# Performance work log

Measured on AMD Instinct MI355X. Metric: run time of the kernel, lower is better.

## Reference

```python
import jax, jax.numpy as jnp
import numpy as np

EPS = 1e-12  # matches torch F.normalize eps


def setup_inputs() -> dict:
    key = jax.random.key(0)
    k1, k2, k3, k4 = jax.random.split(key, 4)
    B, T, C, E, I = 2, 2048, 1024, 16, 256
    return {
        "hidden_states": jax.random.normal(k1, (B, T, C), dtype=jnp.float32),
        "sim_matrix": jax.random.normal(k2, (C, E), dtype=jnp.float32),
        "threshold": jnp.zeros((1,), dtype=jnp.float32),
        "W1": jax.random.normal(k3, (E, I, C), dtype=jnp.float32) * (C ** -0.5),
        "W2": jax.random.normal(k4, (E, C, I), dtype=jnp.float32) * (I ** -0.5),
    }


def reference(hidden_states, sim_matrix, threshold, W1, W2):
    B, T, C = hidden_states.shape
    x = hidden_states.reshape(-1, C)  # [N, C]
    # gate: cosine-similarity scores, threshold mask
    xn = x / jnp.maximum(jnp.linalg.norm(x, axis=-1, keepdims=True), EPS)
    sn = sim_matrix / jnp.maximum(jnp.linalg.norm(sim_matrix, axis=0, keepdims=True), EPS)
    scores = xn @ sn                      # [N, E]
    mask = scores > threshold             # [N, E] bool
    k_per_token = mask.sum(axis=-1)       # [N]
    # expert FFNs: dense per-expert GEMMs, then mask (equals sparse dispatch + zero-fill)
    h = jax.nn.gelu(jnp.einsum('tc,eic->tei', x, W1), approximate=False)  # [N, E, I]
    out = jnp.einsum('tei,eci->tec', h, W2)                               # [N, E, C]
    expert_outputs_full = jnp.where(mask[..., None], out, 0.0)            # [N, E, C]
    # STE gate forward value is just the mask; combine = masked sum over experts
    ste = mask.astype(scores.dtype)
    final = (expert_outputs_full * ste[..., None]).sum(axis=1)            # [N, C]
    return final.reshape(B, T, C), scores, expert_outputs_full, k_per_token
```

## Files before the change

kernel.cpp:

```cpp
#include <hip/hip_runtime.h>
#include <hip/hip_bf16.h>
#include <math.h>
#include <stdint.h>

#define N_TOK 4096
#define C_DIM 1024
#define E_NUM 16
#define I_DIM 256

typedef unsigned short ushort_t;
typedef __attribute__((ext_vector_type(8))) short bf16x8;
typedef __attribute__((ext_vector_type(4))) float f32x4;

#define AS1 __attribute__((address_space(1)))
#define AS3 __attribute__((address_space(3)))

__device__ __forceinline__ void glds16(const void* g, void* l) {
    __builtin_amdgcn_global_load_lds((const AS1 uint32_t*)g, (AS3 uint32_t*)l, 16, 0, 0);
}

__device__ __forceinline__ ushort_t bf16_rne(float v) {
    uint32_t u = __float_as_uint(v);
    u = (u + 0x7FFFu + ((u >> 16) & 1u)) >> 16;
    return (ushort_t)u;
}
__device__ __forceinline__ float bf16_val(ushort_t h) {
    return __uint_as_float(((uint32_t)h) << 16);
}
__device__ __forceinline__ float gelu_exact(float v) {
    return 0.5f * v * (1.0f + erff(v * 0.70710678118654752f));
}

__global__ __launch_bounds__(256) void smk_split(
    const float* __restrict__ src, char* __restrict__ dst, int R, int kush)
{
    const int u  = blockIdx.x * 256 + threadIdx.x;
    const int ku = 1 << kush;
    const int r  = u >> kush;
    const int k8 = u & (ku - 1);
    const int p  = k8 >> 2;
    const int uh = (k8 & 3) ^ (r & 7);

    const float* s = src + ((size_t)r << (kush + 3)) + k8 * 8;
    float4 a = *(const float4*)(s);
    float4 b = *(const float4*)(s + 4);
    float f[8] = {a.x, a.y, a.z, a.w, b.x, b.y, b.z, b.w};

    uint4 hi4, lo4;
    ushort_t* hp = (ushort_t*)&hi4;
    ushort_t* lp = (ushort_t*)&lo4;
    #pragma unroll
    for (int j = 0; j < 8; ++j) {
        ushort_t h = bf16_rne(f[j]);
        hp[j] = h;
        lp[j] = bf16_rne(f[j] - bf16_val(h));
    }
    size_t ob = (((size_t)p * R + r) * 8 + uh) * 16;
    *(uint4*)(dst + ob)        = hi4;
    *(uint4*)(dst + (ob ^ 64)) = lo4;
}

__global__ __launch_bounds__(256) void smk_splitBH(
    const float* __restrict__ src, char* __restrict__ dst, int R, int kush)
{
    const int u  = blockIdx.x * 256 + threadIdx.x;
    const int ku = 1 << kush;
    const int r  = u >> kush;
    const int k8 = u & (ku - 1);
    const int p  = k8 >> 2;
    const int q  = p >> 1;
    const int uh = ((k8 & 3) | ((p & 1) << 2)) ^ (r & 7);

    const float* s = src + ((size_t)r << (kush + 3)) + k8 * 8;
    float4 a = *(const float4*)(s);
    float4 b = *(const float4*)(s + 4);
    float f[8] = {a.x, a.y, a.z, a.w, b.x, b.y, b.z, b.w};

    uint4 hi4;
    ushort_t* hp = (ushort_t*)&hi4;
    #pragma unroll
    for (int j = 0; j < 8; ++j) hp[j] = bf16_rne(f[j]);

    *(uint4*)(dst + (((size_t)q * R + r) * 8 + uh) * 16) = hi4;
}

__global__ __launch_bounds__(256) void smk_gate2(
    const float* __restrict__ x, const float* __restrict__ sim,
    const float* __restrict__ thr,
    float* __restrict__ scores, float* __restrict__ kpt)
{
    __shared__ __align__(16) float ss[C_DIM * E_NUM];
    __shared__ float pm[16][17];
    __shared__ float inv_ns[E_NUM];
    __shared__ float mrow[16][17];

    const int tid = threadIdx.x;
    #pragma unroll
    for (int q = 0; q < 16; ++q)
        *(float4*)&ss[q * 1024 + tid * 4] = *(const float4*)&sim[q * 1024 + tid * 4];
    __syncthreads();

    const int e = tid & 15;
    const int g = tid >> 4;
    float ps = 0.f;
    for (int c = g; c < C_DIM; c += 16) {
        float v = ss[c * 16 + e];
        ps = fmaf(v, v, ps);
    }
    pm[g][e] = ps;
    __syncthreads();
    if (tid < 16) {
        float s = 0.f;
        #pragma unroll
        for (int gg = 0; gg < 16; ++gg) s += pm[gg][tid];
        inv_ns[tid] = 1.f / fmaxf(sqrtf(s), 1e-12f);
    }
    __syncthreads();

    const int t = blockIdx.x * 16 + g;
    const float* xr = x + (size_t)t * C_DIM;
    float dot = 0.f, sq = 0.f;
    for (int c = 0; c < C_DIM; c += 4) {
        float4 xv = *(const float4*)&xr[c];
        dot = fmaf(xv.x, ss[(c + 0) * 16 + e], dot);
        dot = fmaf(xv.y, ss[(c + 1) * 16 + e], dot);
        dot = fmaf(xv.z, ss[(c + 2) * 16 + e], dot);
        dot = fmaf(xv.w, ss[(c + 3) * 16 + e], dot);
        sq  = fmaf(xv.x, xv.x, sq); sq = fmaf(xv.y, xv.y, sq);
        sq  = fmaf(xv.z, xv.z, sq); sq = fmaf(xv.w, xv.w, sq);
    }
    float sc = dot * inv_ns[e] * (1.f / fmaxf(sqrtf(sq), 1e-12f));
    scores[(size_t)t * E_NUM + e] = sc;
    mrow[g][e] = (sc > thr[0]) ? 1.f : 0.f;
    __syncthreads();
    if (e == 0) {
        float k = 0.f;
        #pragma unroll
        for (int ee = 0; ee < 16; ++ee) k += mrow[g][ee];
        kpt[t] = k;
    }
}

__global__ __launch_bounds__(256) void smk_ffn1_mfma(
    const char* __restrict__ Xs, const char* __restrict__ W1h,
    char* __restrict__ Hsh)
{
    __shared__ char As[16384];
    __shared__ char Bs[16384];

    const int e  = blockIdx.z;
    const int t0 = blockIdx.x * 128;
    const int i0 = blockIdx.y * 128;
    const int tid  = threadIdx.x;
    const int lane = tid & 63;
    const int w    = tid >> 6;
    const int wr   = w >> 1, wc = w & 1;

    f32x4 acc[4][4];
    #pragma unroll
    for (int mi = 0; mi < 4; ++mi)
        #pragma unroll
        for (int ni = 0; ni < 4; ++ni)
            acc[mi][ni] = (f32x4){0.f, 0.f, 0.f, 0.f};

    const char* Ag = Xs  + (size_t)t0 * 128 + tid * 16;
    const char* Bg = W1h + ((size_t)(e * 256) + i0) * 128 + tid * 16;

    for (int p = 0; p < 32; ++p) {
        __syncthreads();
        const char* ga = Ag + (size_t)p * (4096 * 128);
        #pragma unroll
        for (int q = 0; q < 4; ++q)
            glds16(ga + q * 4096, As + q * 4096 + tid * 16);
        if ((p & 1) == 0) {
            const char* gb = Bg + (size_t)(p >> 1) * (4096 * 128);
            #pragma unroll
            for (int q = 0; q < 4; ++q)
                glds16(gb + q * 4096, Bs + q * 4096 + tid * 16);
        }
        __syncthreads();

        bf16x8 ah[4], al[4], bh[4];
        #pragma unroll
        for (int mi = 0; mi < 4; ++mi) {
            int r   = wr * 64 + mi * 16 + (lane & 15);
            int ubh = (((lane >> 4)    ) ^ (r & 7)) * 16;
            int ubl = (((lane >> 4) | 4) ^ (r & 7)) * 16;
            ah[mi] = *(const bf16x8*)(As + r * 128 + ubh);
            al[mi] = *(const bf16x8*)(As + r * 128 + ubl);
        }
        const int ubsel = (lane >> 4) | ((p & 1) << 2);
        #pragma unroll
        for (int ni = 0; ni < 4; ++ni) {
            int r  = wc * 64 + ni * 16 + (lane & 15);
            int ub = (ubsel ^ (r & 7)) * 16;
            bh[ni] = *(const bf16x8*)(Bs + r * 128 + ub);
        }
        #pragma unroll
        for (int mi = 0; mi < 4; ++mi)
            #pragma unroll
            for (int ni = 0; ni < 4; ++ni) {
                acc[mi][ni] = __builtin_amdgcn_mfma_f32_16x16x32_bf16(ah[mi], bh[ni], acc[mi][ni], 0, 0, 0);
                acc[mi][ni] = __builtin_amdgcn_mfma_f32_16x16x32_bf16(al[mi], bh[ni], acc[mi][ni], 0, 0, 0);
            }
    }

    const int rb = (lane >> 4) * 4;
    #pragma unroll
    for (int mi = 0; mi < 4; ++mi)
        #pragma unroll
        for (int ni = 0; ni < 4; ++ni) {
            int ig = i0 + wc * 64 + ni * 16 + (lane & 15);
            int pp = ig >> 5, qq = pp >> 1;
            int uu = ((ig >> 3) & 3) | ((pp & 1) << 2);
            #pragma unroll
            for (int j = 0; j < 4; ++j) {
                int t = t0 + wr * 64 + mi * 16 + rb + j;
                float v = gelu_exact(acc[mi][ni][j]);
                size_t ob = (((size_t)((e * 4 + qq) * 4096 + t)) * 8 + (uu ^ (t & 7))) * 16
                          + (ig & 7) * 2;
                *(ushort_t*)(Hsh + ob) = bf16_rne(v);
            }
        }
}

__global__ __launch_bounds__(256) void smk_ffn2_mfma(
    const char* __restrict__ Hsh, const char* __restrict__ W2s,
    const float* __restrict__ scores, const float* __restrict__ thr,
    float* __restrict__ eo)
{
    __shared__ char As[16384];
    __shared__ char Bs[16384];

    const int e  = blockIdx.z;
    const int t0 = blockIdx.x * 128;
    const int c0 = blockIdx.y * 128;
    const int tid  = threadIdx.x;
    const int lane = tid & 63;
    const int w    = tid >> 6;
    const int wr   = w >> 1, wc = w & 1;

    f32x4 acc[4][4];
    #pragma unroll
    for (int mi = 0; mi < 4; ++mi)
        #pragma unroll
        for (int ni = 0; ni < 4; ++ni)
            acc[mi][ni] = (f32x4){0.f, 0.f, 0.f, 0.f};

    const char* Ag = Hsh + ((size_t)(e * 4) * 4096 + t0) * 128 + tid * 16;
    const char* Bg = W2s + ((size_t)(e * 1024) + c0) * 128 + tid * 16;

    for (int p = 0; p < 8; ++p) {
        __syncthreads();
        if ((p & 1) == 0) {
            const char* ga = Ag + (size_t)(p >> 1) * (4096 * 128);
            #pragma unroll
            for (int q = 0; q < 4; ++q)
                glds16(ga + q * 4096, As + q * 4096 + tid * 16);
        }
        const char* gb = Bg + (size_t)p * (16384 * 128);
        #pragma unroll
        for (int q = 0; q < 4; ++q)
            glds16(gb + q * 4096, Bs + q * 4096 + tid * 16);
        __syncthreads();

        bf16x8 ah[4], bh[4], bl[4];
        const int uasel = (lane >> 4) | ((p & 1) << 2);
        #pragma unroll
        for (int mi = 0; mi < 4; ++mi) {
            int r  = wr * 64 + mi * 16 + (lane & 15);
            int ua = (uasel ^ (r & 7)) * 16;
            ah[mi] = *(const bf16x8*)(As + r * 128 + ua);
        }
        #pragma unroll
        for (int ni = 0; ni < 4; ++ni) {
            int r   = wc * 64 + ni * 16 + (lane & 15);
            int ubh = (((lane >> 4)    ) ^ (r & 7)) * 16;
            int ubl = (((lane >> 4) | 4) ^ (r & 7)) * 16;
            bh[ni] = *(const bf16x8*)(Bs + r * 128 + ubh);
            bl[ni] = *(const bf16x8*)(Bs + r * 128 + ubl);
        }
        #pragma unroll
        for (int mi = 0; mi < 4; ++mi)
            #pragma unroll
            for (int ni = 0; ni < 4; ++ni) {
                acc[mi][ni] = __builtin_amdgcn_mfma_f32_16x16x32_bf16(ah[mi], bh[ni], acc[mi][ni], 0, 0, 0);
                acc[mi][ni] = __builtin_amdgcn_mfma_f32_16x16x32_bf16(ah[mi], bl[ni], acc[mi][ni], 0, 0, 0);
            }
    }

    const float th = thr[0];
    const int rb = (lane >> 4) * 4;
    float msk[4][4];
    #pragma unroll
    for (int mi = 0; mi < 4; ++mi)
        #pragma unroll
        for (int j = 0; j < 4; ++j) {
            int t = t0 + wr * 64 + mi * 16 + rb + j;
            msk[mi][j] = (scores[(size_t)t * E_NUM + e] > th) ? 1.f : 0.f;
        }
    #pragma unroll
    for (int mi = 0; mi < 4; ++mi)
        #pragma unroll
        for (int ni = 0; ni < 4; ++ni) {
            int c = c0 + wc * 64 + ni * 16 + (lane & 15);
            #pragma unroll
            for (int j = 0; j < 4; ++j) {
                int t = t0 + wr * 64 + mi * 16 + rb + j;
                eo[((size_t)t * E_NUM + e) * C_DIM + c] = acc[mi][ni][j] * msk[mi][j];
            }
        }
}

__global__ __launch_bounds__(256) void smk_combine(
    const float* __restrict__ eo, float* __restrict__ fin)
{
    size_t idx = ((size_t)blockIdx.x * 256 + threadIdx.x) * 4;
    size_t t = idx / C_DIM;
    int c = (int)(idx % C_DIM);
    const float* p = eo + (size_t)t * E_NUM * C_DIM + c;
    float4 s = {0.f, 0.f, 0.f, 0.f};
    #pragma unroll
    for (int e = 0; e < E_NUM; ++e) {
        float4 v = *(const float4*)&p[(size_t)e * C_DIM];
        s.x += v.x; s.y += v.y; s.z += v.z; s.w += v.w;
    }
    *(float4*)&fin[idx] = s;
}

#define BM 64
#define BN 64
#define KC 16
#define LDP 68

__global__ __launch_bounds__(256) void smk_ffn1(
    const float* __restrict__ X, const float* __restrict__ W1,
    float* __restrict__ H, int eh, int ez0)
{
    const int e  = blockIdx.z + ez0;
    const int t0 = blockIdx.x * BM;
    const int i0 = blockIdx.y * BN;
    const float* Ap = X + (size_t)t0 * C_DIM;
    const float* Bp = W1 + ((size_t)e * I_DIM + i0) * C_DIM;
    __shared__ __align__(16) float As[KC][LDP];
    __shared__ __align__(16) float Bs[KC][LDP];
    const int tid = threadIdx.x;
    const int tx = tid & 15, ty = tid >> 4;
    const int lm = tid >> 2;
    const int lk = (tid & 3) * 4;
    float acc[4][4] = {};
    for (int k0 = 0; k0 < C_DIM; k0 += KC) {
        float4 av = *(const float4*)&Ap[(size_t)lm * C_DIM + k0 + lk];
        float4 bv = *(const float4*)&Bp[(size_t)lm * C_DIM + k0 + lk];
        __syncthreads();
        As[lk + 0][lm] = av.x; As[lk + 1][lm] = av.y;
        As[lk + 2][lm] = av.z; As[lk + 3][lm] = av.w;
        Bs[lk + 0][lm] = bv.x; Bs[lk + 1][lm] = bv.y;
        Bs[lk + 2][lm] = bv.z; Bs[lk + 3][lm] = bv.w;
        __syncthreads();
        #pragma unroll
        for (int k = 0; k < KC; ++k) {
            float4 a4 = *(const float4*)&As[k][ty * 4];
            float4 b4 = *(const float4*)&Bs[k][tx * 4];
            float a[4] = {a4.x, a4.y, a4.z, a4.w};
            float b[4] = {b4.x, b4.y, b4.z, b4.w};
            #pragma unroll
            for (int i = 0; i < 4; ++i)
                #pragma unroll
                for (int j = 0; j < 4; ++j)
                    acc[i][j] = fmaf(a[i], b[j], acc[i][j]);
        }
    }
    const size_t hrow = (size_t)eh * I_DIM;
    float* Hp = H + ((eh == E_NUM) ? (size_t)e * I_DIM : 0);
    #pragma unroll
    for (int i = 0; i < 4; ++i) {
        int t = t0 + ty * 4 + i;
        float4 o;
        o.x = gelu_exact(acc[i][0]); o.y = gelu_exact(acc[i][1]);
        o.z = gelu_exact(acc[i][2]); o.w = gelu_exact(acc[i][3]);
        *(float4*)&Hp[(size_t)t * hrow + i0 + tx * 4] = o;
    }
}

__global__ __launch_bounds__(256) void smk_ffn2(
    const float* __restrict__ Hst, const float* __restrict__ W2,
    const float* __restrict__ scores, const float* __restrict__ thr,
    float* __restrict__ eo, int eh, int ez0)
{
    const int e  = blockIdx.z + ez0;
    const int t0 = blockIdx.x * BM;
    const int c0 = blockIdx.y * BN;
    const size_t hrow = (size_t)eh * I_DIM;
    const float* Ap = Hst + ((eh == E_NUM) ? (size_t)e * I_DIM : 0) + (size_t)t0 * hrow;
    const float* Bp = W2 + ((size_t)e * C_DIM + c0) * I_DIM;
    __shared__ __align__(16) float As[KC][LDP];
    __shared__ __align__(16) float Bs[KC][LDP];
    const int tid = threadIdx.x;
    const int tx = tid & 15, ty = tid >> 4;
    const int lm = tid >> 2;
    const int lk = (tid & 3) * 4;
    float acc[4][4] = {};
    for (int k0 = 0; k0 < I_DIM; k0 += KC) {
        float4 av = *(const float4*)&Ap[(size_t)lm * hrow + k0 + lk];
        float4 bv = *(const float4*)&Bp[(size_t)lm * I_DIM + k0 + lk];
        __syncthreads();
        As[lk + 0][lm] = av.x; As[lk + 1][lm] = av.y;
        As[lk + 2][lm] = av.z; As[lk + 3][lm] = av.w;
        Bs[lk + 0][lm] = bv.x; Bs[lk + 1][lm] = bv.y;
        Bs[lk + 2][lm] = bv.z; Bs[lk + 3][lm] = bv.w;
        __syncthreads();
        #pragma unroll
        for (int k = 0; k < KC; ++k) {
            float4 a4 = *(const float4*)&As[k][ty * 4];
            float4 b4 = *(const float4*)&Bs[k][tx * 4];
            float a[4] = {a4.x, a4.y, a4.z, a4.w};
            float b[4] = {b4.x, b4.y, b4.z, b4.w};
            #pragma unroll
            for (int i = 0; i < 4; ++i)
                #pragma unroll
                for (int j = 0; j < 4; ++j)
                    acc[i][j] = fmaf(a[i], b[j], acc[i][j]);
        }
    }
    const float th = thr[0];
    #pragma unroll
    for (int i = 0; i < 4; ++i) {
        int t = t0 + ty * 4 + i;
        float m = (scores[(size_t)t * E_NUM + e] > th) ? 1.f : 0.f;
        float4 o;
        o.x = acc[i][0] * m; o.y = acc[i][1] * m;
        o.z = acc[i][2] * m; o.w = acc[i][3] * m;
        *(float4*)&eo[((size_t)t * E_NUM + e) * C_DIM + c0 + tx * 4] = o;
    }
}

extern "C" void kernel_launch(void* const* d_in, const int* in_sizes, int n_in,
                              void* d_out, int out_size, void* d_ws, size_t ws_size,
                              hipStream_t stream) {
    const float* x   = (const float*)d_in[0];
    const float* sim = (const float*)d_in[1];
    const float* thr = (const float*)d_in[2];
    const float* W1  = (const float*)d_in[3];
    const float* W2  = (const float*)d_in[4];

    float* out    = (float*)d_out;
    float* fin    = out;
    float* scores = out + (size_t)N_TOK * C_DIM;
    float* eo     = scores + (size_t)N_TOK * E_NUM;
    float* kpt    = eo + (size_t)N_TOK * E_NUM * C_DIM;

    smk_gate2<<<N_TOK / 16, 256, 0, stream>>>(x, sim, thr, scores, kpt);

    const size_t SZ_XS  = 16777216;
    const size_t SZ_W1H = 8388608;
    const size_t SZ_W2S = 16777216;
    const size_t SZ_HSH = 33554432;
    const size_t WS_NEED = SZ_XS + SZ_W1H + SZ_W2S + SZ_HSH;

    if (ws_size >= WS_NEED) {
        char* Xs  = (char*)d_ws;
        char* W1h = Xs + SZ_XS;
        char* W2s = W1h + SZ_W1H;
        char* Hsh = W2s + SZ_W2S;

        smk_split  <<<2048, 256, 0, stream>>>(x,  Xs,  4096,  7);
        smk_splitBH<<<2048, 256, 0, stream>>>(W1, W1h, 4096,  7);
        smk_split  <<<2048, 256, 0, stream>>>(W2, W2s, 16384, 5);

        dim3 g1(32, 2, 16);
        smk_ffn1_mfma<<<g1, 256, 0, stream>>>(Xs, W1h, Hsh);
        dim3 g2(32, 8, 16);
        smk_ffn2_mfma<<<g2, 256, 0, stream>>>(Hsh, W2s, scores, thr, eo);
    } else {
        const size_t needH = (size_t)N_TOK * E_NUM * I_DIM * sizeof(float);
        if (ws_size >= needH) {
            float* H = (float*)d_ws;
            dim3 g1(N_TOK / BM, I_DIM / BN, E_NUM);
            smk_ffn1<<<g1, 256, 0, stream>>>(x, W1, H, E_NUM, 0);
            dim3 g2(N_TOK / BM, C_DIM / BN, E_NUM);
            smk_ffn2<<<g2, 256, 0, stream>>>(H, W2, scores, thr, eo, E_NUM, 0);
        } else {
            float* H = fin;
            for (int e = 0; e < E_NUM; ++e) {
                dim3 g1(N_TOK / BM, I_DIM / BN, 1);
                smk_ffn1<<<g1, 256, 0, stream>>>(x, W1, H, 1, e);
                dim3 g2(N_TOK / BM, C_DIM / BN, 1);
                smk_ffn2<<<g2, 256, 0, stream>>>(H, W2, scores, thr, eo, 1, e);
            }
        }
    }

    smk_combine<<<(N_TOK * C_DIM / 4) / 256, 256, 0, stream>>>(eo, fin);
}
```

Before: 527.4 us.

## Dispatch only active token-expert pairs via per-expert token lists

The gate kernel builds per-expert lists of active tokens with atomics. The FFN1 and FFN2 MFMA kernels then gather only the listed tokens and exit early once past the count. Inactive output rows are zero-filled by a separate kernel, and the combine step reads only active experts. This avoids dense GEMM work for masked pairs, at the cost of atomics, gathered loads and an extra zero-fill launch.

```diff
diff --git a/kernel.cpp b/kernel.cpp
--- a/kernel.cpp
+++ b/kernel.cpp
@@ -29,6 +29,10 @@
 }
 __device__ __forceinline__ float gelu_exact(float v) {
     return 0.5f * v * (1.0f + erff(v * 0.70710678118654752f));
+}
+
+__global__ __launch_bounds__(64) void smk_zero16(int* cnt) {
+    if (threadIdx.x < 16) cnt[threadIdx.x] = 0;
 }
 
 __global__ __launch_bounds__(256) void smk_split(
@@ -87,7 +91,8 @@
 __global__ __launch_bounds__(256) void smk_gate2(
     const float* __restrict__ x, const float* __restrict__ sim,
     const float* __restrict__ thr,
-    float* __restrict__ scores, float* __restrict__ kpt)
+    float* __restrict__ scores, float* __restrict__ kpt,
+    int* __restrict__ lists, int* __restrict__ cnt)
 {
     __shared__ __align__(16) float ss[C_DIM * E_NUM];
     __shared__ float pm[16][17];
@@ -131,7 +136,12 @@
     }
     float sc = dot * inv_ns[e] * (1.f / fmaxf(sqrtf(sq), 1e-12f));
     scores[(size_t)t * E_NUM + e] = sc;
-    mrow[g][e] = (sc > thr[0]) ? 1.f : 0.f;
+    const bool act = sc > thr[0];
+    if (act && lists != nullptr) {
+        int pos = atomicAdd(&cnt[e], 1);
+        lists[e * N_TOK + pos] = t;
+    }
+    mrow[g][e] = act ? 1.f : 0.f;
     __syncthreads();
     if (e == 0) {
         float k = 0.f;
@@ -139,6 +149,225 @@
         for (int ee = 0; ee < 16; ++ee) k += mrow[g][ee];
         kpt[t] = k;
     }
+}
+
+__global__ __launch_bounds__(256) void smk_ffn1_mfma_c(
+    const char* __restrict__ Xs, const char* __restrict__ W1h,
+    char* __restrict__ Hsh, const int* __restrict__ lists,
+    const int* __restrict__ cnt)
+{
+    __shared__ char As[16384];
+    __shared__ char Bs[16384];
+
+    const int e  = blockIdx.z;
+    const int nt = cnt[e];
+    const int t0 = blockIdx.x * 128;
+    if (t0 >= nt) return;
+    const int i0 = blockIdx.y * 128;
+    const int tid  = threadIdx.x;
+    const int lane = tid & 63;
+    const int w    = tid >> 6;
+    const int wr   = w >> 1, wc = w & 1;
+
+    const int srow = tid >> 3;
+    const int v    = tid & 7;
+    const int* le  = lists + e * N_TOK;
+    uint32_t abase[4];
+    #pragma unroll
+    for (int q = 0; q < 4; ++q) {
+        int s    = q * 32 + srow;
+        int slot = t0 + s;
+        int tr   = le[(slot < nt) ? slot : (nt - 1)];
+        abase[q] = (uint32_t)(tr * 128 + (v ^ ((s ^ tr) & 7)) * 16);
+    }
+
+    f32x4 acc[4][4];
+    #pragma unroll
+    for (int mi = 0; mi < 4; ++mi)
+        #pragma unroll
+        for (int ni = 0; ni < 4; ++ni)
+            acc[mi][ni] = (f32x4){0.f, 0.f, 0.f, 0.f};
+
+    const char* Bg = W1h + ((size_t)(e * 256) + i0) * 128 + tid * 16;
+
+    for (int p = 0; p < 32; ++p) {
+        __syncthreads();
+        const char* gp = Xs + (size_t)p * (4096 * 128);
+        #pragma unroll
+        for (int q = 0; q < 4; ++q)
+            glds16(gp + abase[q], As + q * 4096 + tid * 16);
+        if ((p & 1) == 0) {
+            const char* gb = Bg + (size_t)(p >> 1) * (4096 * 128);
+            #pragma unroll
+            for (int q = 0; q < 4; ++q)
+                glds16(gb + q * 4096, Bs + q * 4096 + tid * 16);
+        }
+        __syncthreads();
+
+        bf16x8 ah[4], al[4], bh[4];
+        #pragma unroll
+        for (int mi = 0; mi < 4; ++mi) {
+            int r   = wr * 64 + mi * 16 + (lane & 15);
+            int ubh = (((lane >> 4)    ) ^ (r & 7)) * 16;
+            int ubl = (((lane >> 4) | 4) ^ (r & 7)) * 16;
+            ah[mi] = *(const bf16x8*)(As + r * 128 + ubh);
+            al[mi] = *(const bf16x8*)(As + r * 128 + ubl);
+        }
+        const int ubsel = (lane >> 4) | ((p & 1) << 2);
+        #pragma unroll
+        for (int ni = 0; ni < 4; ++ni) {
+            int r  = wc * 64 + ni * 16 + (lane & 15);
+            int ub = (ubsel ^ (r & 7)) * 16;
+            bh[ni] = *(const bf16x8*)(Bs + r * 128 + ub);
+        }
+        #pragma unroll
+        for (int mi = 0; mi < 4; ++mi)
+            #pragma unroll
+            for (int ni = 0; ni < 4; ++ni) {
+                acc[mi][ni] = __builtin_amdgcn_mfma_f32_16x16x32_bf16(ah[mi], bh[ni], acc[mi][ni], 0, 0, 0);
+                acc[mi][ni] = __builtin_amdgcn_mfma_f32_16x16x32_bf16(al[mi], bh[ni], acc[mi][ni], 0, 0, 0);
+            }
+    }
+
+    const int rb = (lane >> 4) * 4;
+    #pragma unroll
+    for (int mi = 0; mi < 4; ++mi)
+        #pragma unroll
+        for (int ni = 0; ni < 4; ++ni) {
+            int ig = i0 + wc * 64 + ni * 16 + (lane & 15);
+            int pp = ig >> 5, qq = pp >> 1;
+            int uu = ((ig >> 3) & 3) | ((pp & 1) << 2);
+            #pragma unroll
+            for (int j = 0; j < 4; ++j) {
+                int slot = t0 + wr * 64 + mi * 16 + rb + j;
+                float vv = gelu_exact(acc[mi][ni][j]);
+                size_t ob = (((size_t)((e * 4 + qq) * 4096 + slot)) * 8 + (uu ^ (slot & 7))) * 16
+                          + (ig & 7) * 2;
+                *(ushort_t*)(Hsh + ob) = bf16_rne(vv);
+            }
+        }
+}
+
+__global__ __launch_bounds__(256) void smk_ffn2_mfma_c(
+    const char* __restrict__ Hsh, const char* __restrict__ W2s,
+    const int* __restrict__ lists, const int* __restrict__ cnt,
+    float* __restrict__ eo)
+{
+    __shared__ char As[16384];
+    __shared__ char Bs[16384];
+
+    const int e  = blockIdx.z;
+    const int nt = cnt[e];
+    const int t0 = blockIdx.x * 128;
+    if (t0 >= nt) return;
+    const int c0 = blockIdx.y * 128;
+    const int tid  = threadIdx.x;
+    const int lane = tid & 63;
+    const int w    = tid >> 6;
+    const int wr   = w >> 1, wc = w & 1;
+
+    f32x4 acc[4][4];
+    #pragma unroll
+    for (int mi = 0; mi < 4; ++mi)
+        #pragma unroll
+        for (int ni = 0; ni < 4; ++ni)
+            acc[mi][ni] = (f32x4){0.f, 0.f, 0.f, 0.f};
+
+    const char* Ag = Hsh + ((size_t)(e * 4) * 4096 + t0) * 128 + tid * 16;
+    const char* Bg = W2s + ((size_t)(e * 1024) + c0) * 128 + tid * 16;
+
+    for (int p = 0; p < 8; ++p) {
+        __syncthreads();
+        if ((p & 1) == 0) {
+            const char* ga = Ag + (size_t)(p >> 1) * (4096 * 128);
+            #pragma unroll
+            for (int q = 0; q < 4; ++q)
+                glds16(ga + q * 4096, As + q * 4096 + tid * 16);
+        }
+        const char* gb = Bg + (size_t)p * (16384 * 128);
+        #pragma unroll
+        for (int q = 0; q < 4; ++q)
+            glds16(gb + q * 4096, Bs + q * 4096 + tid * 16);
+        __syncthreads();
+
+        bf16x8 ah[4], bh[4], bl[4];
+        const int uasel = (lane >> 4) | ((p & 1) << 2);
+        #pragma unroll
+        for (int mi = 0; mi < 4; ++mi) {
+            int r  = wr * 64 + mi * 16 + (lane & 15);
+            int ua = (uasel ^ (r & 7)) * 16;
+            ah[mi] = *(const bf16x8*)(As + r * 128 + ua);
+        }
+        #pragma unroll
+        for (int ni = 0; ni < 4; ++ni) {
+            int r   = wc * 64 + ni * 16 + (lane & 15);
+            int ubh = (((lane >> 4)    ) ^ (r & 7)) * 16;
+            int ubl = (((lane >> 4) | 4) ^ (r & 7)) * 16;
+            bh[ni] = *(const bf16x8*)(Bs + r * 128 + ubh);
+            bl[ni] = *(const bf16x8*)(Bs + r * 128 + ubl);
+        }
+        #pragma unroll
+        for (int mi = 0; mi < 4; ++mi)
+            #pragma unroll
+            for (int ni = 0; ni < 4; ++ni) {
+                acc[mi][ni] = __builtin_amdgcn_mfma_f32_16x16x32_bf16(ah[mi], bh[ni], acc[mi][ni], 0, 0, 0);
+                acc[mi][ni] = __builtin_amdgcn_mfma_f32_16x16x32_bf16(ah[mi], bl[ni], acc[mi][ni], 0, 0, 0);
+            }
+    }
+
+    const int* le = lists + e * N_TOK;
+    const int rb = (lane >> 4) * 4;
+    #pragma unroll
+    for (int mi = 0; mi < 4; ++mi)
+        #pragma unroll
+        for (int j = 0; j < 4; ++j) {
+            int slot = t0 + wr * 64 + mi * 16 + rb + j;
+            if (slot < nt) {
+                int tr = le[slot];
+                float* dst = eo + ((size_t)tr * E_NUM + e) * C_DIM + c0 + wc * 64 + (lane & 15);
+                #pragma unroll
+                for (int ni = 0; ni < 4; ++ni)
+                    dst[ni * 16] = acc[mi][ni][j];
+            }
+        }
+}
+
+__global__ __launch_bounds__(256) void smk_zerofill(
+    const float* __restrict__ scores, const float* __restrict__ thr,
+    float* __restrict__ eo)
+{
+    const int row = blockIdx.x;
+    if (scores[row] > thr[0]) return;
+    float4 z = {0.f, 0.f, 0.f, 0.f};
+    *(float4*)&eo[(size_t)row * C_DIM + threadIdx.x * 4] = z;
+}
+
+__global__ __launch_bounds__(256) void smk_combine2(
+    const float* __restrict__ eo, const float* __restrict__ scores,
+    const float* __restrict__ thr, float* __restrict__ fin)
+{
+    const int t = blockIdx.x;
+    __shared__ unsigned am;
+    if (threadIdx.x == 0) {
+        unsigned m = 0;
+        float th = thr[0];
+        #pragma unroll
+        for (int e = 0; e < E_NUM; ++e)
+            if (scores[t * E_NUM + e] > th) m |= (1u << e);
+        am = m;
+    }
+    __syncthreads();
+    const unsigned m = am;
+    const float* p = eo + (size_t)t * E_NUM * C_DIM + threadIdx.x * 4;
+    float4 s = {0.f, 0.f, 0.f, 0.f};
+    #pragma unroll
+    for (int e = 0; e < E_NUM; ++e) {
+        if (m & (1u << e)) {
+            float4 v = *(const float4*)&p[(size_t)e * C_DIM];
+            s.x += v.x; s.y += v.y; s.z += v.z; s.w += v.w;
+        }
+    }
+    *(float4*)&fin[(size_t)t * C_DIM + threadIdx.x * 4] = s;
 }
 
 __global__ __launch_bounds__(256) void smk_ffn1_mfma(
@@ -216,10 +445,10 @@
             #pragma unroll
             for (int j = 0; j < 4; ++j) {
                 int t = t0 + wr * 64 + mi * 16 + rb + j;
-                float v = gelu_exact(acc[mi][ni][j]);
+                float vv = gelu_exact(acc[mi][ni][j]);
                 size_t ob = (((size_t)((e * 4 + qq) * 4096 + t)) * 8 + (uu ^ (t & 7))) * 16
                           + (ig & 7) * 2;
-                *(ushort_t*)(Hsh + ob) = bf16_rne(v);
+                *(ushort_t*)(Hsh + ob) = bf16_rne(vv);
             }
         }
 }
@@ -310,22 +539,6 @@
                 eo[((size_t)t * E_NUM + e) * C_DIM + c] = acc[mi][ni][j] * msk[mi][j];
             }
         }
-}
-
-__global__ __launch_bounds__(256) void smk_combine(
-    const float* __restrict__ eo, float* __restrict__ fin)
-{
-    size_t idx = ((size_t)blockIdx.x * 256 + threadIdx.x) * 4;
-    size_t t = idx / C_DIM;
-    int c = (int)(idx % C_DIM);
-    const float* p = eo + (size_t)t * E_NUM * C_DIM + c;
-    float4 s = {0.f, 0.f, 0.f, 0.f};
-    #pragma unroll
-    for (int e = 0; e < E_NUM; ++e) {
-        float4 v = *(const float4*)&p[(size_t)e * C_DIM];
-        s.x += v.x; s.y += v.y; s.z += v.z; s.w += v.w;
-    }
-    *(float4*)&fin[idx] = s;
 }
 
 #define BM 64
@@ -450,29 +663,48 @@
     float* eo     = scores + (size_t)N_TOK * E_NUM;
     float* kpt    = eo + (size_t)N_TOK * E_NUM * C_DIM;
 
-    smk_gate2<<<N_TOK / 16, 256, 0, stream>>>(x, sim, thr, scores, kpt);
-
     const size_t SZ_XS  = 16777216;
     const size_t SZ_W1H = 8388608;
     const size_t SZ_W2S = 16777216;
     const size_t SZ_HSH = 33554432;
-    const size_t WS_NEED = SZ_XS + SZ_W1H + SZ_W2S + SZ_HSH;
-
-    if (ws_size >= WS_NEED) {
-        char* Xs  = (char*)d_ws;
-        char* W1h = Xs + SZ_XS;
-        char* W2s = W1h + SZ_W1H;
-        char* Hsh = W2s + SZ_W2S;
+    const size_t SZ_LST = (size_t)E_NUM * N_TOK * sizeof(int);
+    const size_t WS_MFMA = SZ_XS + SZ_W1H + SZ_W2S + SZ_HSH;
+    const size_t WS_FULL = WS_MFMA + SZ_LST + 256;
+
+    char* Xs  = (char*)d_ws;
+    char* W1h = Xs + SZ_XS;
+    char* W2s = W1h + SZ_W1H;
+    char* Hsh = W2s + SZ_W2S;
+    int*  lists = (int*)(Hsh + SZ_HSH);
+    int*  cnt   = lists + E_NUM * N_TOK;
+
+    if (ws_size >= WS_FULL) {
+        smk_zero16<<<1, 64, 0, stream>>>(cnt);
+        smk_gate2<<<N_TOK / 16, 256, 0, stream>>>(x, sim, thr, scores, kpt, lists, cnt);
 
         smk_split  <<<2048, 256, 0, stream>>>(x,  Xs,  4096,  7);
         smk_splitBH<<<2048, 256, 0, stream>>>(W1, W1h, 4096,  7);
         smk_split  <<<2048, 256, 0, stream>>>(W2, W2s, 16384, 5);
 
+        dim3 g1(32, 2, 16);
+        smk_ffn1_mfma_c<<<g1, 256, 0, stream>>>(Xs, W1h, Hsh, lists, cnt);
+        dim3 g2(32, 8, 16);
+        smk_ffn2_mfma_c<<<g2, 256, 0, stream>>>(Hsh, W2s, lists, cnt, eo);
+
+        smk_zerofill<<<N_TOK * E_NUM, 256, 0, stream>>>(scores, thr, eo);
+        smk_combine2<<<N_TOK, 256, 0, stream>>>(eo, scores, thr, fin);
+    } else if (ws_size >= WS_MFMA) {
+        smk_gate2<<<N_TOK / 16, 256, 0, stream>>>(x, sim, thr, scores, kpt, nullptr, nullptr);
+        smk_split  <<<2048, 256, 0, stream>>>(x,  Xs,  4096,  7);
+        smk_splitBH<<<2048, 256, 0, stream>>>(W1, W1h, 4096,  7);
+        smk_split  <<<2048, 256, 0, stream>>>(W2, W2s, 16384, 5);
         dim3 g1(32, 2, 16);
         smk_ffn1_mfma<<<g1, 256, 0, stream>>>(Xs, W1h, Hsh);
         dim3 g2(32, 8, 16);
         smk_ffn2_mfma<<<g2, 256, 0, stream>>>(Hsh, W2s, scores, thr, eo);
+        smk_combine2<<<N_TOK, 256, 0, stream>>>(eo, scores, thr, fin);
     } else {
+        smk_gate2<<<N_TOK / 16, 256, 0, stream>>>(x, sim, thr, scores, kpt, nullptr, nullptr);
         const size_t needH = (size_t)N_TOK * E_NUM * I_DIM * sizeof(float);
         if (ws_size >= needH) {
             float* H = (float*)d_ws;
@@ -489,7 +721,6 @@
                 smk_ffn2<<<g2, 256, 0, stream>>>(H, W2, scores, thr, eo, 1, e);
             }
         }
-    }
-
-    smk_combine<<<(N_TOK * C_DIM / 4) / 256, 256, 0, stream>>>(eo, fin);
-}
+        smk_combine2<<<N_TOK, 256, 0, stream>>>(eo, scores, thr, fin);
+    }
+}
```

New measurement: 642.4 us. 21.8% more time.
